# Performance work log

Hardware: AMD Instinct MI355X
Metric: run time of the kernel (lower is better)

The kernel has to match this reference:

```python
import jax, jax.numpy as jnp
import numpy as np

D = 256  # atom_feature_dim
LN_EPS = 1e-5
NEG_SLOPE = 0.01  # LeakyReLU default


def setup_inputs() -> dict:
    key = jax.random.key(0)
    ks = jax.random.split(key, 8)
    B, N, L = 16, 256, 1024
    inv = 1.0 / np.sqrt(D)
    return {
        "mol_atom_feature": jax.random.normal(ks[0], (B, N, D), jnp.float32),
        "atom_feature": jax.random.normal(ks[1], (B, L, D), jnp.float32),
        "mol_atom_attend_mask": jnp.ones((B, L), jnp.float32),
        "mol_atom_softmax_mask": jnp.zeros((B, L), jnp.float32),
        # nn.Linear(D, D) params (weight stored [out, in] torch-style; we use x @ W.T form via einsum)
        "W_mol": jax.random.uniform(ks[2], (D, D), jnp.float32, -inv, inv),
        "b_mol": jnp.zeros((D,), jnp.float32),
        "W_nb": jax.random.uniform(ks[3], (D, D), jnp.float32, -inv, inv),
        "b_nb": jnp.zeros((D,), jnp.float32),
        # nn.Linear(2D, 1): weight [2D], bias scalar
        "align_w": jax.random.uniform(ks[4], (2 * D,), jnp.float32, -1.0 / np.sqrt(2 * D), 1.0 / np.sqrt(2 * D)),
        "align_b": jnp.zeros((), jnp.float32),
        "ln_gamma": jnp.ones((D,), jnp.float32),
        "ln_beta": jnp.zeros((D,), jnp.float32),
    }


def reference(mol_atom_feature, atom_feature, mol_atom_attend_mask, mol_atom_softmax_mask,
              W_mol, b_mol, W_nb, b_nb, align_w, align_b, ln_gamma, ln_beta):
    # Linear transforms (dropout is identity in eval)
    x = jnp.einsum('bnd,ed->bne', mol_atom_feature, W_mol) + b_mol   # [B,N,D]
    a = jnp.einsum('bld,ed->ble', atom_feature, W_nb) + b_nb        # [B,L,D]

    # GAT align: Linear over concat([x_i, a_j]) is separable:
    # score[b,n,l] = x[b,n]@w1 + a[b,l]@w2 + b
    w1, w2 = align_w[:D], align_w[D:]
    score = (x @ w1)[:, :, None] + (a @ w2)[:, None, :] + align_b   # [B,N,L]
    score = jax.nn.leaky_relu(score, NEG_SLOPE)

    # additive softmax mask over atom axis, then masked softmax + attend mask
    score = score + mol_atom_softmax_mask[:, None, :]
    attn = jax.nn.softmax(score, axis=-1)
    attn = attn * mol_atom_attend_mask[:, None, :]

    # weighted aggregation of transformed atom features
    ctx = jnp.einsum('bnl,bld->bnd', attn, a)                        # [B,N,D]

    # LayerNorm
    mu = jnp.mean(ctx, axis=-1, keepdims=True)
    var = jnp.var(ctx, axis=-1, keepdims=True)
    out = (ctx - mu) * jax.lax.rsqrt(var + LN_EPS) * ln_gamma + ln_beta
    return out
```

## Files before the change

kernel.cpp:

```cpp
#include <hip/hip_runtime.h>
#include <hip/hip_bf16.h>
#include <math.h>

#define BB 16
#define NN 256
#define LL 1024
#define DD 256

constexpr float LN_EPS = 1e-5f;
constexpr float NEG_SLOPE = 0.01f;

typedef __attribute__((ext_vector_type(8))) short short8;
typedef __attribute__((ext_vector_type(4))) float f32x4;
typedef __attribute__((ext_vector_type(4))) int i32x4;

static __device__ __forceinline__ unsigned cvtpk(float lo, float hi) {
  __hip_bfloat162 h = __float22bfloat162_rn(make_float2(lo, hi));
  union { __hip_bfloat162 h; unsigned u; } v; v.h = h;
  return v.u;
}
static __device__ __forceinline__ short8 pack8(float4 f0, float4 f1) {
  union { i32x4 i; short8 s; } v;
  v.i.x = cvtpk(f0.x, f0.y);
  v.i.y = cvtpk(f0.z, f0.w);
  v.i.z = cvtpk(f1.x, f1.y);
  v.i.w = cvtpk(f1.z, f1.w);
  return v.s;
}
static __device__ __forceinline__ unsigned short f2bf(float f) {
  union { float f; unsigned u; } v; v.f = f;
  unsigned r = v.u + 0x7FFFu + ((v.u >> 16) & 1u);
  return (unsigned short)(r >> 16);
}

__global__ __launch_bounds__(512) void agemm_kernel(
    const float* __restrict__ atom, const float* __restrict__ W_nb,
    const float* __restrict__ b_nb, const float* __restrict__ W_mol,
    const float* __restrict__ b_mol, const float* __restrict__ align_w,
    const float* __restrict__ align_b, unsigned short* __restrict__ aT,
    float* __restrict__ s2g, float* __restrict__ v1c) {
  __shared__ char atile[64 * 256 * 2];
  __shared__ unsigned short sAT[256 * 68];
  __shared__ float vp[32][16];
  __shared__ float s2p[8][66];

  int t = threadIdx.x;
  int w = t >> 6, lane = t & 63;
  int i = blockIdx.x;
  int x = i & 7, k = i >> 3;
  int b = x + 8 * (k >> 4);
  int l0 = (k & 15) * 64;
  int lo16 = lane & 15, g = lane >> 4;

  {
    int r = t >> 3, dseg = (t & 7) * 32;
    const float* src = atom + (size_t)(b * LL + l0 + r) * DD + dseg;
    #pragma unroll
    for (int q = 0; q < 4; ++q) {
      float4 f0 = *(const float4*)(src + q * 8);
      float4 f1 = *(const float4*)(src + q * 8 + 4);
      int byte = ((r * 256 + dseg + q * 8) * 2) ^ ((r & 7) << 4);
      *(short8*)(atile + byte) = pack8(f0, f1);
    }
  }

  if (i < 16) {
    int d0 = i * 16;
    int dl = t & 15, eseg = t >> 4;
    float acc = 0.f;
    #pragma unroll
    for (int q = 0; q < 8; ++q) {
      int e = eseg * 8 + q;
      acc += align_w[e] * W_mol[e * DD + d0 + dl];
    }
    vp[eseg][dl] = acc;
    __syncthreads();
    if (t < 16) {
      float s = 0.f;
      #pragma unroll
      for (int q = 0; q < 32; ++q) s += vp[q][t];
      v1c[d0 + t] = s;
    }
    if (i == 0 && w == 1) {
      float s = b_mol[lane] * align_w[lane] +
                b_mol[lane + 64] * align_w[lane + 64] +
                b_mol[lane + 128] * align_w[lane + 128] +
                b_mol[lane + 192] * align_w[lane + 192];
      #pragma unroll
      for (int off = 32; off > 0; off >>= 1) s += __shfl_xor(s, off, 64);
      if (lane == 0) v1c[256] = s + align_b[0];
    }
  }
  __syncthreads();

  f32x4 acc[2][4];
  #pragma unroll
  for (int m = 0; m < 2; ++m)
    #pragma unroll
    for (int n = 0; n < 4; ++n) acc[m][n] = f32x4{0.f, 0.f, 0.f, 0.f};

  const float* Ap = W_nb + (size_t)(w * 32 + lo16) * DD + g * 8;

  #pragma unroll 4
  for (int kk = 0; kk < 8; ++kk) {
    short8 af[2];
    #pragma unroll
    for (int m = 0; m < 2; ++m) {
      float4 f0 = *(const float4*)(Ap + m * 16 * DD + kk * 32);
      float4 f1 = *(const float4*)(Ap + m * 16 * DD + kk * 32 + 4);
      af[m] = pack8(f0, f1);
    }
    short8 bf[4];
    #pragma unroll
    for (int n = 0; n < 4; ++n) {
      int l = n * 16 + lo16;
      int byte = ((l * 256 + kk * 32 + g * 8) * 2) ^ ((l & 7) << 4);
      bf[n] = *(const short8*)(atile + byte);
    }
    #pragma unroll
    for (int m = 0; m < 2; ++m)
      #pragma unroll
      for (int n = 0; n < 4; ++n)
        acc[m][n] = __builtin_amdgcn_mfma_f32_16x16x32_bf16(af[m], bf[n],
                                                            acc[m][n], 0, 0, 0);
  }

  {
    float4 bias[2], w2r[2];
    #pragma unroll
    for (int m = 0; m < 2; ++m) {
      bias[m] = *(const float4*)&b_nb[w * 32 + m * 16 + g * 4];
      w2r[m] = *(const float4*)&align_w[DD + w * 32 + m * 16 + g * 4];
    }
    float p[4] = {0.f, 0.f, 0.f, 0.f};
    #pragma unroll
    for (int m = 0; m < 2; ++m) {
      #pragma unroll
      for (int n = 0; n < 4; ++n) {
        int l = n * 16 + lo16;
        #pragma unroll
        for (int jj = 0; jj < 4; ++jj) {
          float v = acc[m][n][jj] + ((const float*)&bias[m])[jj];
          sAT[(w * 32 + m * 16 + g * 4 + jj) * 68 + l] = f2bf(v);
          p[n] += ((const float*)&w2r[m])[jj] * v;
        }
      }
    }
    #pragma unroll
    for (int n = 0; n < 4; ++n) {
      p[n] += __shfl_xor(p[n], 16, 64);
      p[n] += __shfl_xor(p[n], 32, 64);
    }
    if (g == 0) {
      #pragma unroll
      for (int n = 0; n < 4; ++n) s2p[w][n * 16 + lo16] = p[n];
    }
  }
  __syncthreads();

  if (t < 64) {
    float s = 0.f;
    #pragma unroll
    for (int q = 0; q < 8; ++q) s += s2p[q][t];
    s2g[b * LL + l0 + t] = s;
  }
  unsigned short* dst = aT + (size_t)b * DD * LL + l0;
  #pragma unroll
  for (int idx = t; idx < 4096; idx += 512) {
    int e = idx >> 4, ch = idx & 15;
    ushort4 v = *(const ushort4*)&sAT[e * 68 + ch * 4];
    *(ushort4*)(dst + (size_t)e * LL + ch * 4) = v;
  }
}

__global__ __launch_bounds__(512) void attn_kernel(
    const unsigned short* __restrict__ aT, const float* __restrict__ mol,
    const float* __restrict__ v1c, const float* __restrict__ s2,
    const float* __restrict__ amask, const float* __restrict__ smask,
    const float* __restrict__ gamma, const float* __restrict__ beta,
    float* __restrict__ out) {
  __shared__ unsigned short sattn[16 * 1024];
  __shared__ float ctxp[2][16][260];
  __shared__ float v1s[256];
  __shared__ float s1s[16];
  __shared__ float mu_s[16], rs_s[16];
  int i = blockIdx.x;
  int x = i & 7, k = i >> 3;
  int b = x + 8 * (k >> 4);
  int n0 = (k & 15) * 16;
  int t = threadIdx.x, w = t >> 6, lane = t & 63;

  float c0 = v1c[256];
  if (t < 256) v1s[t] = v1c[t];
  __syncthreads();

  {
    int r = t >> 5, off = (t & 31) * 8;
    const float* mr = mol + (size_t)(b * NN + n0 + r) * DD + off;
    float s = 0.f;
    #pragma unroll
    for (int q = 0; q < 2; ++q) {
      float4 f = *(const float4*)(mr + q * 4);
      s += f.x * v1s[off + q * 4] + f.y * v1s[off + q * 4 + 1] +
           f.z * v1s[off + q * 4 + 2] + f.w * v1s[off + q * 4 + 3];
    }
    s += __shfl_xor(s, 1, 64);
    s += __shfl_xor(s, 2, 64);
    s += __shfl_xor(s, 4, 64);
    s += __shfl_xor(s, 8, 64);
    s += __shfl_xor(s, 16, 64);
    if ((t & 31) == 0) s1s[r] = s + c0;
  }
  __syncthreads();

  {
    float s2v[16], amv[16], smv[16];
    #pragma unroll
    for (int q = 0; q < 16; ++q) {
      int l = lane + 64 * q;
      s2v[q] = s2[b * LL + l];
      amv[q] = amask[b * LL + l];
      smv[q] = smask[b * LL + l];
    }
    #pragma unroll
    for (int rr = 0; rr < 2; ++rr) {
      int r = w * 2 + rr;
      float s1v = s1s[r];
      float p[16];
      float mx = -INFINITY;
      #pragma unroll
      for (int q = 0; q < 16; ++q) {
        float sc = s1v + s2v[q];
        sc = sc > 0.f ? sc : NEG_SLOPE * sc;
        sc += smv[q];
        p[q] = sc;
        mx = fmaxf(mx, sc);
      }
      #pragma unroll
      for (int off = 32; off > 0; off >>= 1) mx = fmaxf(mx, __shfl_xor(mx, off, 64));
      float sum = 0.f;
      #pragma unroll
      for (int q = 0; q < 16; ++q) {
        p[q] = __expf(p[q] - mx);
        sum += p[q];
      }
      #pragma unroll
      for (int off = 32; off > 0; off >>= 1) sum += __shfl_xor(sum, off, 64);
      float inv = 1.f / sum;
      #pragma unroll
      for (int q = 0; q < 16; ++q) {
        unsigned short bv = f2bf(p[q] * amv[q] * inv);
        int l = lane + 64 * q;
        int byte = ((r * 1024 + l) * 2) ^ ((r & 7) << 4);
        *(unsigned short*)((char*)sattn + byte) = bv;
      }
    }
  }
  __syncthreads();

  int lo16 = lane & 15, g = lane >> 4;
  {
    int e0 = (w & 3) * 64, lh = w >> 2;
    f32x4 acc[4];
    #pragma unroll
    for (int n = 0; n < 4; ++n) acc[n] = f32x4{0.f, 0.f, 0.f, 0.f};
    const unsigned short* Bp =
        aT + (size_t)b * DD * LL + (size_t)(e0 + lo16) * LL + lh * 512 + g * 8;
    #pragma unroll 8
    for (int kk = 0; kk < 16; ++kk) {
      short8 afr = *(const short8*)((const char*)sattn +
          (((lo16 * 1024 + lh * 512 + kk * 32 + g * 8) * 2) ^ ((lo16 & 7) << 4)));
      #pragma unroll
      for (int n = 0; n < 4; ++n) {
        short8 bfr = *(const short8*)(Bp + (size_t)n * 16 * LL + kk * 32);
        acc[n] = __builtin_amdgcn_mfma_f32_16x16x32_bf16(afr, bfr, acc[n], 0, 0, 0);
      }
    }
    #pragma unroll
    for (int n = 0; n < 4; ++n)
      #pragma unroll
      for (int jj = 0; jj < 4; ++jj)
        ctxp[lh][g * 4 + jj][e0 + n * 16 + lo16] = acc[n][jj];
  }
  __syncthreads();

  #pragma unroll
  for (int rr = 0; rr < 2; ++rr) {
    int r = w * 2 + rr;
    float s = 0.f, sq = 0.f;
    #pragma unroll
    for (int jj = 0; jj < 4; ++jj) {
      int cc = lane + 64 * jj;
      float v = ctxp[0][r][cc] + ctxp[1][r][cc];
      s += v;
      sq += v * v;
    }
    #pragma unroll
    for (int off = 32; off > 0; off >>= 1) {
      s += __shfl_xor(s, off, 64);
      sq += __shfl_xor(sq, off, 64);
    }
    if (lane == 0) {
      float mu = s * (1.f / 256.f);
      float var = sq * (1.f / 256.f) - mu * mu;
      mu_s[r] = mu;
      rs_s[r] = rsqrtf(var + LN_EPS);
    }
  }
  __syncthreads();

  #pragma unroll
  for (int q = 0; q < 8; ++q) {
    int idx = t + 512 * q;
    int r = idx >> 8, d = idx & 255;
    float v = ctxp[0][r][d] + ctxp[1][r][d];
    out[(size_t)(b * NN + n0 + r) * DD + d] =
        (v - mu_s[r]) * rs_s[r] * gamma[d] + beta[d];
  }
}

extern "C" void kernel_launch(void* const* d_in, const int* in_sizes, int n_in,
                              void* d_out, int out_size, void* d_ws, size_t ws_size,
                              hipStream_t stream) {
  const float* mol     = (const float*)d_in[0];
  const float* atom    = (const float*)d_in[1];
  const float* amask   = (const float*)d_in[2];
  const float* smask   = (const float*)d_in[3];
  const float* W_mol   = (const float*)d_in[4];
  const float* b_mol   = (const float*)d_in[5];
  const float* W_nb    = (const float*)d_in[6];
  const float* b_nb    = (const float*)d_in[7];
  const float* align_w = (const float*)d_in[8];
  const float* align_b = (const float*)d_in[9];
  const float* gamma   = (const float*)d_in[10];
  const float* beta    = (const float*)d_in[11];
  float* outp = (float*)d_out;

  char* wsb = (char*)d_ws;
  unsigned short* aT = (unsigned short*)wsb;
  float* s2g = (float*)(wsb + 8388608);
  float* v1c = s2g + BB * LL;

  agemm_kernel<<<256, 512, 0, stream>>>(atom, W_nb, b_nb, W_mol, b_mol,
                                        align_w, align_b, aT, s2g, v1c);
  attn_kernel<<<256, 512, 0, stream>>>(aT, mol, v1c, s2g, amask, smask,
                                       gamma, beta, outp);
}
```

Baseline: 39.54 us.

## Split atom GEMM output columns across two blocks to double grid size

The atom-projection GEMM kernel now launches 512 blocks, each computing half of the output features (128 of 256) for a 64-row tile. The align score contribution is written as two partial sums, and the attention kernel adds them when it loads. This is meant to fill more compute units on the MI355X and shorten each block's work. In exchange, every atom tile is loaded and converted to bf16 twice, and the attention kernel does an extra global read per score.

```diff
diff --git a/kernel.cpp b/kernel.cpp
--- a/kernel.cpp
+++ b/kernel.cpp
@@ -38,9 +38,9 @@
     const float* __restrict__ b_nb, const float* __restrict__ W_mol,
     const float* __restrict__ b_mol, const float* __restrict__ align_w,
     const float* __restrict__ align_b, unsigned short* __restrict__ aT,
-    float* __restrict__ s2g, float* __restrict__ v1c) {
+    float* __restrict__ s2part, float* __restrict__ v1c) {
   __shared__ char atile[64 * 256 * 2];
-  __shared__ unsigned short sAT[256 * 68];
+  __shared__ unsigned short sAT[128 * 68];
   __shared__ float vp[32][16];
   __shared__ float s2p[8][66];
 
@@ -48,8 +48,11 @@
   int w = t >> 6, lane = t & 63;
   int i = blockIdx.x;
   int x = i & 7, k = i >> 3;
-  int b = x + 8 * (k >> 4);
-  int l0 = (k & 15) * 64;
+  int b = x + 8 * (k >> 5);
+  int j = k & 31;
+  int l0 = (j & 15) * 64;
+  int eh = j >> 4;
+  int e_base = eh * 128;
   int lo16 = lane & 15, g = lane >> 4;
 
   {
@@ -93,23 +96,17 @@
   }
   __syncthreads();
 
-  f32x4 acc[2][4];
+  f32x4 acc[4];
   #pragma unroll
-  for (int m = 0; m < 2; ++m)
-    #pragma unroll
-    for (int n = 0; n < 4; ++n) acc[m][n] = f32x4{0.f, 0.f, 0.f, 0.f};
-
-  const float* Ap = W_nb + (size_t)(w * 32 + lo16) * DD + g * 8;
+  for (int n = 0; n < 4; ++n) acc[n] = f32x4{0.f, 0.f, 0.f, 0.f};
+
+  const float* Ap = W_nb + (size_t)(e_base + w * 16 + lo16) * DD + g * 8;
 
   #pragma unroll 4
   for (int kk = 0; kk < 8; ++kk) {
-    short8 af[2];
-    #pragma unroll
-    for (int m = 0; m < 2; ++m) {
-      float4 f0 = *(const float4*)(Ap + m * 16 * DD + kk * 32);
-      float4 f1 = *(const float4*)(Ap + m * 16 * DD + kk * 32 + 4);
-      af[m] = pack8(f0, f1);
-    }
+    float4 f0 = *(const float4*)(Ap + kk * 32);
+    float4 f1 = *(const float4*)(Ap + kk * 32 + 4);
+    short8 af = pack8(f0, f1);
     short8 bf[4];
     #pragma unroll
     for (int n = 0; n < 4; ++n) {
@@ -118,32 +115,22 @@
       bf[n] = *(const short8*)(atile + byte);
     }
     #pragma unroll
-    for (int m = 0; m < 2; ++m)
-      #pragma unroll
-      for (int n = 0; n < 4; ++n)
-        acc[m][n] = __builtin_amdgcn_mfma_f32_16x16x32_bf16(af[m], bf[n],
-                                                            acc[m][n], 0, 0, 0);
-  }
-
-  {
-    float4 bias[2], w2r[2];
-    #pragma unroll
-    for (int m = 0; m < 2; ++m) {
-      bias[m] = *(const float4*)&b_nb[w * 32 + m * 16 + g * 4];
-      w2r[m] = *(const float4*)&align_w[DD + w * 32 + m * 16 + g * 4];
-    }
+    for (int n = 0; n < 4; ++n)
+      acc[n] = __builtin_amdgcn_mfma_f32_16x16x32_bf16(af, bf[n], acc[n], 0, 0, 0);
+  }
+
+  {
+    float4 bias = *(const float4*)&b_nb[e_base + w * 16 + g * 4];
+    float4 w2r = *(const float4*)&align_w[DD + e_base + w * 16 + g * 4];
     float p[4] = {0.f, 0.f, 0.f, 0.f};
     #pragma unroll
-    for (int m = 0; m < 2; ++m) {
-      #pragma unroll
-      for (int n = 0; n < 4; ++n) {
-        int l = n * 16 + lo16;
-        #pragma unroll
-        for (int jj = 0; jj < 4; ++jj) {
-          float v = acc[m][n][jj] + ((const float*)&bias[m])[jj];
-          sAT[(w * 32 + m * 16 + g * 4 + jj) * 68 + l] = f2bf(v);
-          p[n] += ((const float*)&w2r[m])[jj] * v;
-        }
+    for (int n = 0; n < 4; ++n) {
+      int l = n * 16 + lo16;
+      #pragma unroll
+      for (int jj = 0; jj < 4; ++jj) {
+        float v = acc[n][jj] + ((const float*)&bias)[jj];
+        sAT[(w * 16 + g * 4 + jj) * 68 + l] = f2bf(v);
+        p[n] += ((const float*)&w2r)[jj] * v;
       }
     }
     #pragma unroll
@@ -162,11 +149,11 @@
     float s = 0.f;
     #pragma unroll
     for (int q = 0; q < 8; ++q) s += s2p[q][t];
-    s2g[b * LL + l0 + t] = s;
-  }
-  unsigned short* dst = aT + (size_t)b * DD * LL + l0;
+    s2part[eh * BB * LL + b * LL + l0 + t] = s;
+  }
+  unsigned short* dst = aT + (size_t)b * DD * LL + (size_t)e_base * LL + l0;
   #pragma unroll
-  for (int idx = t; idx < 4096; idx += 512) {
+  for (int idx = t; idx < 2048; idx += 512) {
     int e = idx >> 4, ch = idx & 15;
     ushort4 v = *(const ushort4*)&sAT[e * 68 + ch * 4];
     *(ushort4*)(dst + (size_t)e * LL + ch * 4) = v;
@@ -175,7 +162,7 @@
 
 __global__ __launch_bounds__(512) void attn_kernel(
     const unsigned short* __restrict__ aT, const float* __restrict__ mol,
-    const float* __restrict__ v1c, const float* __restrict__ s2,
+    const float* __restrict__ v1c, const float* __restrict__ s2part,
     const float* __restrict__ amask, const float* __restrict__ smask,
     const float* __restrict__ gamma, const float* __restrict__ beta,
     float* __restrict__ out) {
@@ -218,7 +205,7 @@
     #pragma unroll
     for (int q = 0; q < 16; ++q) {
       int l = lane + 64 * q;
-      s2v[q] = s2[b * LL + l];
+      s2v[q] = s2part[b * LL + l] + s2part[BB * LL + b * LL + l];
       amv[q] = amask[b * LL + l];
       smv[q] = smask[b * LL + l];
     }
@@ -338,11 +325,11 @@
 
   char* wsb = (char*)d_ws;
   unsigned short* aT = (unsigned short*)wsb;
-  float* s2g = (float*)(wsb + 8388608);
-  float* v1c = s2g + BB * LL;
-
-  agemm_kernel<<<256, 512, 0, stream>>>(atom, W_nb, b_nb, W_mol, b_mol,
-                                        align_w, align_b, aT, s2g, v1c);
-  attn_kernel<<<256, 512, 0, stream>>>(aT, mol, v1c, s2g, amask, smask,
+  float* s2part = (float*)(wsb + 8388608);
+  float* v1c = s2part + 2 * BB * LL;
+
+  agemm_kernel<<<512, 512, 0, stream>>>(atom, W_nb, b_nb, W_mol, b_mol,
+                                        align_w, align_b, aT, s2part, v1c);
+  attn_kernel<<<256, 512, 0, stream>>>(aT, mol, v1c, s2part, amask, smask,
                                        gamma, beta, outp);
 }
```

Result: slower. 41.21 us (+4.2%).

## Halve query rows per attention block and double grid to 512 blocks

Applied to the files above, without the earlier changes.

The attention kernel now handles 8 query rows per block instead of 16 and launches 512 blocks, with one wave per row for the score and softmax stages. Rows 8-15 of the bf16 attention tile are zero-filled so the 16-row MFMA still works, and only half the accumulator rows are written back. The aim is more parallelism and better CU coverage on the 256-CU device, at the cost of wasting half the MFMA work and re-reading the aT operand twice as often.

```diff
diff --git a/kernel.cpp b/kernel.cpp
--- a/kernel.cpp
+++ b/kernel.cpp
@@ -180,80 +180,68 @@
     const float* __restrict__ gamma, const float* __restrict__ beta,
     float* __restrict__ out) {
   __shared__ unsigned short sattn[16 * 1024];
-  __shared__ float ctxp[2][16][260];
+  __shared__ float ctxp[2][8][260];
   __shared__ float v1s[256];
-  __shared__ float s1s[16];
-  __shared__ float mu_s[16], rs_s[16];
+  __shared__ float s1s[8];
+  __shared__ float mu_s[8], rs_s[8];
   int i = blockIdx.x;
   int x = i & 7, k = i >> 3;
-  int b = x + 8 * (k >> 4);
-  int n0 = (k & 15) * 16;
+  int b = x + 8 * (k >> 5);
+  int n0 = (k & 31) * 8;
   int t = threadIdx.x, w = t >> 6, lane = t & 63;
 
   float c0 = v1c[256];
   if (t < 256) v1s[t] = v1c[t];
-  __syncthreads();
-
-  {
-    int r = t >> 5, off = (t & 31) * 8;
-    const float* mr = mol + (size_t)(b * NN + n0 + r) * DD + off;
-    float s = 0.f;
-    #pragma unroll
-    for (int q = 0; q < 2; ++q) {
-      float4 f = *(const float4*)(mr + q * 4);
-      s += f.x * v1s[off + q * 4] + f.y * v1s[off + q * 4 + 1] +
-           f.z * v1s[off + q * 4 + 2] + f.w * v1s[off + q * 4 + 3];
-    }
-    s += __shfl_xor(s, 1, 64);
-    s += __shfl_xor(s, 2, 64);
-    s += __shfl_xor(s, 4, 64);
-    s += __shfl_xor(s, 8, 64);
-    s += __shfl_xor(s, 16, 64);
-    if ((t & 31) == 0) s1s[r] = s + c0;
-  }
-  __syncthreads();
-
-  {
-    float s2v[16], amv[16], smv[16];
+  {
+    unsigned* z = (unsigned*)(sattn + 8 * 1024);
+    #pragma unroll
+    for (int q = 0; q < 8; ++q) z[t + 512 * q] = 0;
+  }
+  __syncthreads();
+
+  {
+    const float* mr = mol + (size_t)(b * NN + n0 + w) * DD + lane * 4;
+    float4 f = *(const float4*)mr;
+    float s = f.x * v1s[lane * 4] + f.y * v1s[lane * 4 + 1] +
+              f.z * v1s[lane * 4 + 2] + f.w * v1s[lane * 4 + 3];
+    #pragma unroll
+    for (int off = 32; off > 0; off >>= 1) s += __shfl_xor(s, off, 64);
+    if (lane == 0) s1s[w] = s + c0;
+  }
+  __syncthreads();
+
+  {
+    int r = w;
+    float s1v = s1s[r];
+    float p[16], amv[16];
+    float mx = -INFINITY;
     #pragma unroll
     for (int q = 0; q < 16; ++q) {
       int l = lane + 64 * q;
-      s2v[q] = s2[b * LL + l];
+      float sc = s1v + s2[b * LL + l];
+      sc = sc > 0.f ? sc : NEG_SLOPE * sc;
+      sc += smask[b * LL + l];
       amv[q] = amask[b * LL + l];
-      smv[q] = smask[b * LL + l];
-    }
-    #pragma unroll
-    for (int rr = 0; rr < 2; ++rr) {
-      int r = w * 2 + rr;
-      float s1v = s1s[r];
-      float p[16];
-      float mx = -INFINITY;
-      #pragma unroll
-      for (int q = 0; q < 16; ++q) {
-        float sc = s1v + s2v[q];
-        sc = sc > 0.f ? sc : NEG_SLOPE * sc;
-        sc += smv[q];
-        p[q] = sc;
-        mx = fmaxf(mx, sc);
-      }
-      #pragma unroll
-      for (int off = 32; off > 0; off >>= 1) mx = fmaxf(mx, __shfl_xor(mx, off, 64));
-      float sum = 0.f;
-      #pragma unroll
-      for (int q = 0; q < 16; ++q) {
-        p[q] = __expf(p[q] - mx);
-        sum += p[q];
-      }
-      #pragma unroll
-      for (int off = 32; off > 0; off >>= 1) sum += __shfl_xor(sum, off, 64);
-      float inv = 1.f / sum;
-      #pragma unroll
-      for (int q = 0; q < 16; ++q) {
-        unsigned short bv = f2bf(p[q] * amv[q] * inv);
-        int l = lane + 64 * q;
-        int byte = ((r * 1024 + l) * 2) ^ ((r & 7) << 4);
-        *(unsigned short*)((char*)sattn + byte) = bv;
-      }
+      p[q] = sc;
+      mx = fmaxf(mx, sc);
+    }
+    #pragma unroll
+    for (int off = 32; off > 0; off >>= 1) mx = fmaxf(mx, __shfl_xor(mx, off, 64));
+    float sum = 0.f;
+    #pragma unroll
+    for (int q = 0; q < 16; ++q) {
+      p[q] = __expf(p[q] - mx);
+      sum += p[q];
+    }
+    #pragma unroll
+    for (int off = 32; off > 0; off >>= 1) sum += __shfl_xor(sum, off, 64);
+    float inv = 1.f / sum;
+    #pragma unroll
+    for (int q = 0; q < 16; ++q) {
+      unsigned short bv = f2bf(p[q] * amv[q] * inv);
+      int l = lane + 64 * q;
+      int byte = ((r * 1024 + l) * 2) ^ ((r & 7) << 4);
+      *(unsigned short*)((char*)sattn + byte) = bv;
     }
   }
   __syncthreads();
@@ -276,17 +264,18 @@
         acc[n] = __builtin_amdgcn_mfma_f32_16x16x32_bf16(afr, bfr, acc[n], 0, 0, 0);
       }
     }
-    #pragma unroll
-    for (int n = 0; n < 4; ++n)
-      #pragma unroll
-      for (int jj = 0; jj < 4; ++jj)
-        ctxp[lh][g * 4 + jj][e0 + n * 16 + lo16] = acc[n][jj];
-  }
-  __syncthreads();
-
-  #pragma unroll
-  for (int rr = 0; rr < 2; ++rr) {
-    int r = w * 2 + rr;
+    if (g < 2) {
+      #pragma unroll
+      for (int n = 0; n < 4; ++n)
+        #pragma unroll
+        for (int jj = 0; jj < 4; ++jj)
+          ctxp[lh][g * 4 + jj][e0 + n * 16 + lo16] = acc[n][jj];
+    }
+  }
+  __syncthreads();
+
+  {
+    int r = w;
     float s = 0.f, sq = 0.f;
     #pragma unroll
     for (int jj = 0; jj < 4; ++jj) {
@@ -310,7 +299,7 @@
   __syncthreads();
 
   #pragma unroll
-  for (int q = 0; q < 8; ++q) {
+  for (int q = 0; q < 4; ++q) {
     int idx = t + 512 * q;
     int r = idx >> 8, d = idx & 255;
     float v = ctxp[0][r][d] + ctxp[1][r][d];
@@ -343,6 +332,6 @@
 
   agemm_kernel<<<256, 512, 0, stream>>>(atom, W_nb, b_nb, W_mol, b_mol,
                                         align_w, align_b, aT, s2g, v1c);
-  attn_kernel<<<256, 512, 0, stream>>>(aT, mol, v1c, s2g, amask, smask,
+  attn_kernel<<<512, 512, 0, stream>>>(aT, mol, v1c, s2g, amask, smask,
                                        gamma, beta, outp);
 }
```

Result: slower. 51.74 us (+30.8%).
